# Kernel optimization log

Measured on AMD Instinct MI355X. Metric: run time of the kernel, lower is better.

## Reference

```python
import jax, jax.numpy as jnp
import numpy as np

K = 3        # kernel_size
GROUP = 32   # group
EPS = 1e-5   # BatchNorm eps


def setup_inputs() -> dict:
    key = jax.random.key(0)
    k1, k2 = jax.random.split(key)
    x = jax.random.normal(k1, (4, 256, 128, 128), jnp.float32)
    conv_w = jax.random.normal(k2, (GROUP * K * K, 256, K, K), jnp.float32) * 0.05
    gamma = jnp.ones((GROUP * K * K,), jnp.float32)
    beta = jnp.zeros((GROUP * K * K,), jnp.float32)
    return {"x": x, "conv_w": conv_w, "gamma": gamma, "beta": beta}


def _bilinear_align_corners(x, H, W):
    # F.upsample(..., mode='bilinear', align_corners=True)
    n, c, h, w = x.shape
    ys = jnp.linspace(0.0, h - 1.0, H)
    xs = jnp.linspace(0.0, w - 1.0, W)
    y0 = jnp.floor(ys).astype(jnp.int32)
    x0 = jnp.floor(xs).astype(jnp.int32)
    y1 = jnp.minimum(y0 + 1, h - 1)
    x1 = jnp.minimum(x0 + 1, w - 1)
    wy = (ys - y0)[None, None, :, None]
    wx = (xs - x0)[None, None, None, :]
    rows0 = x[:, :, y0, :]
    rows1 = x[:, :, y1, :]
    top = rows0[:, :, :, x0] * (1 - wx) + rows0[:, :, :, x1] * wx
    bot = rows1[:, :, :, x0] * (1 - wx) + rows1[:, :, :, x1] * wx
    return top * (1 - wy) + bot * wy


def reference(x, conv_w, gamma, beta):
    n, c, h0, w0 = x.shape
    # sigma = softmax(BN(conv(x))) over the full G*K*K channel dim
    sigma = jax.lax.conv_general_dilated(
        x, conv_w, (1, 1), 'VALID', dimension_numbers=('NCHW', 'OIHW', 'NCHW'))
    mean = sigma.mean(axis=(0, 2, 3))
    var = sigma.var(axis=(0, 2, 3))  # biased, matches BN training mode
    sigma = (sigma - mean[None, :, None, None]) * jax.lax.rsqrt(var + EPS)[None, :, None, None]
    sigma = sigma * gamma[None, :, None, None] + beta[None, :, None, None]
    sigma = jax.nn.softmax(sigma, axis=1)  # (n, G*K*K, h, w)
    h, w = sigma.shape[2], sigma.shape[3]  # h = h0-K+1, w = w0-K+1
    # Unfold: patches (n, c, K*K, h, w) with channel outer, kernel-pos inner (torch F.unfold order)
    patches = jnp.stack([x[:, :, i:i + h, j:j + w]
                         for i in range(K) for j in range(K)], axis=2)
    patches = patches.reshape(n, GROUP, c // GROUP, K * K, h, w)
    sig = sigma.reshape(n, GROUP, K * K, h, w)
    # Per-pixel, per-group weighted sum over the K*K window
    out = jnp.einsum('ngcphw,ngphw->ngchw', patches, sig).reshape(n, c, h, w)
    return _bilinear_align_corners(out, h0, w0)
```

## Files before the change

### kernel.cpp

```cpp
#include <hip/hip_runtime.h>
#include <hip/hip_bf16.h>
#include <math.h>

#define N 4
#define C 256
#define H 128
#define W 128
#define CO 288
#define OH 126
#define OW 126
#define GROUP 32
#define CPG 8
#define EPS 1e-5f

#define HW (OH*OW)
#define XSLICE (H*W)
#define XNSTRIDE (C*H*W)
#define SNSTRIDE (CO*HW)
#define LONSTRIDE (C*HW)
#define WSTRIDE (CO*256)
#define WTOT (9*CO*256)
#define XTOT (N*H*W*C)

typedef unsigned short u16;
typedef __attribute__((ext_vector_type(8))) short short8;
typedef __attribute__((ext_vector_type(4))) float float4v;

__device__ inline u16 f2bf(float v) {
    __hip_bfloat16 b = __float2bfloat16(v);
    return __builtin_bit_cast(u16, b);
}
__device__ inline float bf2f(u16 u) {
    __hip_bfloat16 b = __builtin_bit_cast(__hip_bfloat16, u);
    return __bfloat162float(b);
}

__global__ __launch_bounds__(256) void split_x_kernel(const float* __restrict__ x,
                                                      u16* __restrict__ xh,
                                                      u16* __restrict__ xl) {
    const int ci = threadIdx.x;
    const int w0 = blockIdx.x * 8;
    const int h  = blockIdx.y;
    const int n  = blockIdx.z;
    const float* src = x + ((size_t)(n*C + ci)*H + h)*W + w0;
    float4 v0 = *(const float4*)src;
    float4 v1 = *(const float4*)(src + 4);
    float vals[8] = {v0.x, v0.y, v0.z, v0.w, v1.x, v1.y, v1.z, v1.w};
    size_t obase = ((size_t)(n*H + h)*W + w0)*C + ci;
    #pragma unroll
    for (int dw = 0; dw < 8; ++dw) {
        float v = vals[dw];
        u16 hb = f2bf(v);
        xh[obase + (size_t)dw*C] = hb;
        xl[obase + (size_t)dw*C] = f2bf(v - bf2f(hb));
    }
}

__global__ __launch_bounds__(256) void split_w_kernel(const float* __restrict__ wgt,
                                                      u16* __restrict__ whT,
                                                      u16* __restrict__ wlT) {
    const int i = blockIdx.x*256 + threadIdx.x;
    const int ci = i & 255;
    const int co = (i >> 8) % CO;
    const int s  = i / (CO*256);
    float v = wgt[(size_t)co*(C*9) + (size_t)ci*9 + s];
    u16 hb = f2bf(v);
    whT[i] = hb;
    wlT[i] = f2bf(v - bf2f(hb));
}

__global__ __launch_bounds__(256, 2) void conv_mfma_kernel(const u16* __restrict__ xh,
                                                           const u16* __restrict__ whT,
                                                           float* __restrict__ sigma) {
    __shared__ __align__(16) u16 xs[8*4*66*8];
    __shared__ __align__(16) u16 wsh[2*4*288*8];

    const int tid  = threadIdx.x;
    const int wave = tid >> 6;
    const int lane = tid & 63;
    const int m16  = lane & 15;
    const int q    = lane >> 4;
    const int wr   = wave & 1;
    const int wc   = wave >> 1;
    const int ow0  = blockIdx.x * 64;
    const int oh0  = blockIdx.y * 2;
    const int n    = blockIdx.z;

    const int bid = blockIdx.x + 2*(blockIdx.y + 63*blockIdx.z);
    if (bid & 1) __builtin_amdgcn_s_sleep(40);

    const int w_nw   = (wave < 2) ? 5 : 4;
    const int w_base = (wave < 2) ? wave*320 : 640 + (wave-2)*256;
    int wsrc[5];
    #pragma unroll
    for (int i = 0; i < 5; ++i) {
        int c = w_base + i*64 + lane;
        const int cq  = c / 288;
        const int cco = c - cq*288;
        wsrc[i] = cco*256 + cq*8;
    }

    int xoff[9];
    #pragma unroll
    for (int t = 0; t < 9; ++t) {
        int c = (4*t + wave)*64 + lane;
        if (c > 2111) c = 2111;
        const int spq = c / 264;
        const int rem = c - spq*264;
        const int row = rem / 66;
        const int col = rem - row*66;
        int gc = ow0 + col; if (gc > W-1) gc = W-1;
        xoff[t] = (spq >> 2)*XTOT + ((n*H + oh0 + row)*W + gc)*C + (spq & 3)*8;
    }

    const int aoff = (q*264 + wr*66 + m16)*8;
    const int boff = (q*288 + wc*144 + m16)*8;

    float4v acc[4][9];
    #pragma unroll
    for (int mt = 0; mt < 4; ++mt)
        #pragma unroll
        for (int j = 0; j < 9; ++j) acc[mt][j] = (float4v)(0.f);

    #pragma unroll
    for (int t = 0; t < 9; ++t)
        if (t < 8 || wave == 0)
            __builtin_amdgcn_global_load_lds((const uint*)(xh + xoff[t]),
                                             (uint*)(xs + (4*t + wave)*512), 16, 0, 0);
    #pragma unroll
    for (int i = 0; i < 5; ++i)
        if (i < w_nw)
            __builtin_amdgcn_global_load_lds((const uint*)(whT + wsrc[i]),
                                             (uint*)(wsh + (w_base + i*64)*8), 16, 0, 0);
    __syncthreads();

    int buf = 0;
    for (int ci0 = 0; ci0 < C; ci0 += 32) {
        #pragma unroll
        for (int ky = 0; ky < 3; ++ky)
        #pragma unroll
        for (int kx = 0; kx < 3; ++kx) {
            const int s = ky*3 + kx;

            {
                const int soff = WTOT + s*WSTRIDE + ci0;
                #pragma unroll
                for (int i = 0; i < 5; ++i)
                    if (i < w_nw)
                        __builtin_amdgcn_global_load_lds(
                            (const uint*)(whT + soff + wsrc[i]),
                            (uint*)(wsh + ((buf^1)*1152 + w_base + i*64)*8), 16, 0, 0);
            }
            const int ab = aoff + (ky*66 + kx)*8;
            short8 ah0 = *(const short8*)&xs[ab];
            short8 ah1 = *(const short8*)&xs[ab + 128];
            short8 ah2 = *(const short8*)&xs[ab + 256];
            short8 ah3 = *(const short8*)&xs[ab + 384];
            {
                short8 al0 = *(const short8*)&xs[ab + 8448];
                short8 al1 = *(const short8*)&xs[ab + 8448 + 128];
                short8 al2 = *(const short8*)&xs[ab + 8448 + 256];
                short8 al3 = *(const short8*)&xs[ab + 8448 + 384];
                const u16* wb = wsh + buf*9216 + boff;
                __builtin_amdgcn_s_setprio(1);
                #pragma unroll
                for (int j = 0; j < 9; ++j) {
                    short8 bh = *(const short8*)&wb[j*128];
                    acc[0][j] = __builtin_amdgcn_mfma_f32_16x16x32_bf16(ah0, bh, acc[0][j], 0, 0, 0);
                    acc[1][j] = __builtin_amdgcn_mfma_f32_16x16x32_bf16(ah1, bh, acc[1][j], 0, 0, 0);
                    acc[2][j] = __builtin_amdgcn_mfma_f32_16x16x32_bf16(ah2, bh, acc[2][j], 0, 0, 0);
                    acc[3][j] = __builtin_amdgcn_mfma_f32_16x16x32_bf16(ah3, bh, acc[3][j], 0, 0, 0);
                    acc[0][j] = __builtin_amdgcn_mfma_f32_16x16x32_bf16(al0, bh, acc[0][j], 0, 0, 0);
                    acc[1][j] = __builtin_amdgcn_mfma_f32_16x16x32_bf16(al1, bh, acc[1][j], 0, 0, 0);
                    acc[2][j] = __builtin_amdgcn_mfma_f32_16x16x32_bf16(al2, bh, acc[2][j], 0, 0, 0);
                    acc[3][j] = __builtin_amdgcn_mfma_f32_16x16x32_bf16(al3, bh, acc[3][j], 0, 0, 0);
                }
                __builtin_amdgcn_s_setprio(0);
            }
            __syncthreads();
            buf ^= 1;

            if (!(ci0 == C-32 && s == 8)) {
                int ns = s + 1, nci = ci0;
                if (ns == 9) { ns = 0; nci += 32; }
                const int soff = ns*WSTRIDE + nci;
                #pragma unroll
                for (int i = 0; i < 5; ++i)
                    if (i < w_nw)
                        __builtin_amdgcn_global_load_lds(
                            (const uint*)(whT + soff + wsrc[i]),
                            (uint*)(wsh + ((buf^1)*1152 + w_base + i*64)*8), 16, 0, 0);
                if (s == 8) {
                    #pragma unroll
                    for (int t = 0; t < 9; ++t)
                        if (t < 8 || wave == 0)
                            __builtin_amdgcn_global_load_lds(
                                (const uint*)(xh + xoff[t] + nci),
                                (uint*)(xs + (4*t + wave)*512), 16, 0, 0);
                }
            }
            {
                const u16* wb = wsh + buf*9216 + boff;
                __builtin_amdgcn_s_setprio(1);
                #pragma unroll
                for (int j = 0; j < 9; ++j) {
                    short8 bl = *(const short8*)&wb[j*128];
                    acc[0][j] = __builtin_amdgcn_mfma_f32_16x16x32_bf16(ah0, bl, acc[0][j], 0, 0, 0);
                    acc[1][j] = __builtin_amdgcn_mfma_f32_16x16x32_bf16(ah1, bl, acc[1][j], 0, 0, 0);
                    acc[2][j] = __builtin_amdgcn_mfma_f32_16x16x32_bf16(ah2, bl, acc[2][j], 0, 0, 0);
                    acc[3][j] = __builtin_amdgcn_mfma_f32_16x16x32_bf16(ah3, bl, acc[3][j], 0, 0, 0);
                }
                __builtin_amdgcn_s_setprio(0);
            }
            __syncthreads();
            buf ^= 1;
        }
    }

    #pragma unroll
    for (int mt = 0; mt < 4; ++mt) {
        const int posb = mt*16 + q*4;
        #pragma unroll
        for (int j = 0; j < 9; ++j) {
            const int co = wc*144 + j*16 + m16;
            float* dst = sigma + (size_t)n*SNSTRIDE + (size_t)co*HW + (oh0 + wr)*OW;
            #pragma unroll
            for (int r = 0; r < 4; ++r) {
                const int ow = ow0 + posb + r;
                if (ow < OW) dst[ow] = acc[mt][j][r];
            }
        }
    }
}

__global__ __launch_bounds__(1024) void stats_kernel(const float* __restrict__ sigma,
                                                     const float* __restrict__ gamma,
                                                     const float* __restrict__ beta,
                                                     float* __restrict__ coef) {
    const int c = blockIdx.x;
    float sum = 0.f, sq = 0.f;
    for (int n = 0; n < N; ++n) {
        const float* sp = sigma + (size_t)n*SNSTRIDE + (size_t)c*HW;
        for (int i = threadIdx.x; i < HW; i += 1024) {
            float v = sp[i];
            sum += v; sq += v * v;
        }
    }
    for (int off = 32; off > 0; off >>= 1) {
        sum += __shfl_down(sum, off, 64);
        sq  += __shfl_down(sq,  off, 64);
    }
    __shared__ float ls[16], lq[16];
    const int wid = threadIdx.x >> 6, lane = threadIdx.x & 63;
    if (lane == 0) { ls[wid] = sum; lq[wid] = sq; }
    __syncthreads();
    if (threadIdx.x == 0) {
        float S = 0.f, Q = 0.f;
        #pragma unroll
        for (int i = 0; i < 16; ++i) { S += ls[i]; Q += lq[i]; }
        const float cnt = (float)(N * HW);
        float mean = S / cnt;
        float var  = Q / cnt - mean * mean;
        float a = gamma[c] * rsqrtf(var + EPS);
        coef[c]      = a;
        coef[CO + c] = beta[c] - mean * a;
    }
}

__global__ __launch_bounds__(256) void fuse_kernel(const float* __restrict__ x,
                                                   const float* __restrict__ sigma,
                                                   const float* __restrict__ coef,
                                                   float* __restrict__ outlo,
                                                   float* __restrict__ sums) {
    __shared__ float a[CO], b[CO];
    for (int i = threadIdx.x; i < CO; i += 256) {
        a[i] = coef[i];
        b[i] = coef[CO + i];
    }
    __syncthreads();

    const int t4 = blockIdx.x * 256 + threadIdx.x;
    if (t4 >= N * HW * 4) return;
    const int gpos = t4 >> 2;
    const int gc   = t4 & 3;
    const int n  = gpos / HW;
    const int hw = gpos - n * HW;
    const int oh = hw / OW;
    const int ow = hw - oh * OW;

    const float* sp = sigma + (size_t)n * SNSTRIDE + hw;
    const float* xb = x + (size_t)n * XNSTRIDE + oh * W + ow;
    float* ob = outlo + (size_t)n * LONSTRIDE + hw;

    float sum = 0.f;
    for (int gl = 0; gl < 8; ++gl) {
        const int g = gc * 8 + gl;
        float acc[CPG];
        #pragma unroll
        for (int c = 0; c < CPG; ++c) acc[c] = 0.f;
        #pragma unroll
        for (int p = 0; p < 9; ++p) {
            const int ch = g * 9 + p;
            float s = sp[(size_t)ch * HW] * a[ch] + b[ch];
            float e = __expf(s);
            sum += e;
            const float* xr = xb + (size_t)(g * CPG) * XSLICE + (p / 3) * W + (p % 3);
            #pragma unroll
            for (int c = 0; c < CPG; ++c)
                acc[c] += xr[(size_t)c * XSLICE] * e;
        }
        #pragma unroll
        for (int c = 0; c < CPG; ++c)
            ob[(size_t)(g * CPG + c) * HW] = acc[c];
    }
    sum += __shfl_xor(sum, 1, 64);
    sum += __shfl_xor(sum, 2, 64);
    if (gc == 0) sums[gpos] = sum;
}

__global__ __launch_bounds__(256) void upsample_kernel(const float* __restrict__ lo,
                                                       const float* __restrict__ sums,
                                                       float* __restrict__ out) {
    const int idx = blockIdx.x * 256 + threadIdx.x;
    const int xi = idx & (W - 1);
    const int yi = (idx >> 7) & (H - 1);
    const int nc = idx >> 14;
    const int n  = nc >> 8;

    const float scale = 125.0f / 127.0f;
    const float sy = yi * scale;
    const float sx = xi * scale;
    int y0 = (int)sy;
    int x0 = (int)sx;
    float wy = sy - (float)y0;
    float wx = sx - (float)x0;
    int y1 = min(y0 + 1, OH - 1);
    int x1 = min(x0 + 1, OW - 1);

    const float* p  = lo + (size_t)nc * HW;
    const float* ps = sums + (size_t)n * HW;
    float v00 = p[y0 * OW + x0] / ps[y0 * OW + x0];
    float v01 = p[y0 * OW + x1] / ps[y0 * OW + x1];
    float v10 = p[y1 * OW + x0] / ps[y1 * OW + x0];
    float v11 = p[y1 * OW + x1] / ps[y1 * OW + x1];
    float top = v00 * (1.f - wx) + v01 * wx;
    float bot = v10 * (1.f - wx) + v11 * wx;
    out[idx] = top * (1.f - wy) + bot * wy;
}

extern "C" void kernel_launch(void* const* d_in, const int* in_sizes, int n_in,
                              void* d_out, int out_size, void* d_ws, size_t ws_size,
                              hipStream_t stream) {
    const float* x      = (const float*)d_in[0];
    const float* conv_w = (const float*)d_in[1];
    const float* gamma  = (const float*)d_in[2];
    const float* beta   = (const float*)d_in[3];
    float* out = (float*)d_out;
    float* ws  = (float*)d_ws;

    float* sigma = ws;
    float* coef  = ws + 18289152;
    float* outlo = ws + 18290176;
    u16* xhp = (u16*)(ws + 18290176);
    u16* xlp = xhp + (size_t)XTOT;
    u16* whT = xlp + (size_t)XTOT;
    u16* wlT = whT + (size_t)WTOT;
    float* sums = (float*)whT;

    split_x_kernel<<<dim3(16, 128, 4), 256, 0, stream>>>(x, xhp, xlp);
    split_w_kernel<<<(9*CO*256)/256, 256, 0, stream>>>(conv_w, whT, wlT);

    conv_mfma_kernel<<<dim3(2, 63, N), 256, 0, stream>>>(xhp, whT, sigma);

    stats_kernel<<<CO, 1024, 0, stream>>>(sigma, gamma, beta, coef);

    fuse_kernel<<<(N * HW * 4 + 255) / 256, 256, 0, stream>>>(x, sigma, coef, outlo, sums);

    upsample_kernel<<<(N * C * H * W) / 256, 256, 0, stream>>>(outlo, sums, out);
}
```

Measured before the change: 614.8 us.

## Enlarge conv tile to four output rows with 512-thread blocks and merged weight staging

The conv MFMA kernel now uses 8 waves per block and covers 4 output rows instead of 2, so each weight tile staged in LDS is reused across twice as many pixels. The weight hi and lo halves are loaded together into one larger double buffer, which cuts the barriers per kernel tap from two to one. The tap loop is no longer unrolled, and the staggered s_sleep start is dropped. In exchange the kernel needs much more LDS per block (about 125 KB), which limits occupancy. Padded rows are clamped on load and skipped on store.

```diff
diff --git a/kernel.cpp b/kernel.cpp
--- a/kernel.cpp
+++ b/kernel.cpp
@@ -69,51 +69,51 @@
     wlT[i] = f2bf(v - bf2f(hb));
 }
 
-__global__ __launch_bounds__(256, 2) void conv_mfma_kernel(const u16* __restrict__ xh,
+__global__ __launch_bounds__(512, 2) void conv_mfma_kernel(const u16* __restrict__ xh,
                                                            const u16* __restrict__ whT,
                                                            float* __restrict__ sigma) {
-    __shared__ __align__(16) u16 xs[8*4*66*8];
-    __shared__ __align__(16) u16 wsh[2*4*288*8];
+    __shared__ __align__(16) u16 xs[25600];
+    __shared__ __align__(16) u16 wsh[2*18432];
 
     const int tid  = threadIdx.x;
     const int wave = tid >> 6;
     const int lane = tid & 63;
     const int m16  = lane & 15;
     const int q    = lane >> 4;
-    const int wr   = wave & 1;
-    const int wc   = wave >> 1;
+    const int wr   = wave & 3;
+    const int wc   = wave >> 2;
     const int ow0  = blockIdx.x * 64;
-    const int oh0  = blockIdx.y * 2;
+    const int oh0  = blockIdx.y * 4;
     const int n    = blockIdx.z;
 
-    const int bid = blockIdx.x + 2*(blockIdx.y + 63*blockIdx.z);
-    if (bid & 1) __builtin_amdgcn_s_sleep(40);
-
-    const int w_nw   = (wave < 2) ? 5 : 4;
-    const int w_base = (wave < 2) ? wave*320 : 640 + (wave-2)*256;
+    const int w_n    = (wave < 4) ? 5 : 4;
+    const int w_base = (wave < 4) ? wave*320 : 1280 + (wave-4)*256;
     int wsrc[5];
     #pragma unroll
     for (int i = 0; i < 5; ++i) {
         int c = w_base + i*64 + lane;
-        const int cq  = c / 288;
-        const int cco = c - cq*288;
-        wsrc[i] = cco*256 + cq*8;
-    }
-
-    int xoff[9];
-    #pragma unroll
-    for (int t = 0; t < 9; ++t) {
-        int c = (4*t + wave)*64 + lane;
-        if (c > 2111) c = 2111;
-        const int spq = c / 264;
-        const int rem = c - spq*264;
+        const int sp  = c / 1152;
+        const int rem = c - sp*1152;
+        const int qc  = rem / 288;
+        const int co  = rem - qc*288;
+        wsrc[i] = sp*WTOT + co*256 + qc*8;
+    }
+
+    int xoff[7];
+    #pragma unroll
+    for (int t = 0; t < 7; ++t) {
+        int c = (8*t + wave)*64 + lane;
+        if (c > 3167) c = 3167;
+        const int spq = c / 396;
+        const int rem = c - spq*396;
         const int row = rem / 66;
         const int col = rem - row*66;
+        int gr = oh0 + row; if (gr > H-1) gr = H-1;
         int gc = ow0 + col; if (gc > W-1) gc = W-1;
-        xoff[t] = (spq >> 2)*XTOT + ((n*H + oh0 + row)*W + gc)*C + (spq & 3)*8;
-    }
-
-    const int aoff = (q*264 + wr*66 + m16)*8;
+        xoff[t] = (spq >> 2)*XTOT + ((n*H + gr)*W + gc)*C + (spq & 3)*8;
+    }
+
+    const int aoff = (q*396 + wr*66 + m16)*8;
     const int boff = (q*288 + wc*144 + m16)*8;
 
     float4v acc[4][9];
@@ -123,111 +123,105 @@
         for (int j = 0; j < 9; ++j) acc[mt][j] = (float4v)(0.f);
 
     #pragma unroll
-    for (int t = 0; t < 9; ++t)
-        if (t < 8 || wave == 0)
+    for (int t = 0; t < 7; ++t)
+        if (t < 6 || wave < 2)
             __builtin_amdgcn_global_load_lds((const uint*)(xh + xoff[t]),
-                                             (uint*)(xs + (4*t + wave)*512), 16, 0, 0);
+                                             (uint*)(xs + (8*t + wave)*512), 16, 0, 0);
     #pragma unroll
     for (int i = 0; i < 5; ++i)
-        if (i < w_nw)
+        if (i < w_n)
             __builtin_amdgcn_global_load_lds((const uint*)(whT + wsrc[i]),
                                              (uint*)(wsh + (w_base + i*64)*8), 16, 0, 0);
     __syncthreads();
 
     int buf = 0;
     for (int ci0 = 0; ci0 < C; ci0 += 32) {
-        #pragma unroll
-        for (int ky = 0; ky < 3; ++ky)
-        #pragma unroll
-        for (int kx = 0; kx < 3; ++kx) {
-            const int s = ky*3 + kx;
-
-            {
-                const int soff = WTOT + s*WSTRIDE + ci0;
+        #pragma unroll 1
+        for (int s = 0; s < 9; ++s) {
+            if (s < 8) {
+                const int soff = (s+1)*WSTRIDE + ci0;
                 #pragma unroll
                 for (int i = 0; i < 5; ++i)
-                    if (i < w_nw)
+                    if (i < w_n)
                         __builtin_amdgcn_global_load_lds(
                             (const uint*)(whT + soff + wsrc[i]),
-                            (uint*)(wsh + ((buf^1)*1152 + w_base + i*64)*8), 16, 0, 0);
-            }
+                            (uint*)(wsh + ((buf^1)*18432 + (w_base + i*64)*8)), 16, 0, 0);
+            }
+
+            const int ky = s / 3;
+            const int kx = s - 3*ky;
             const int ab = aoff + (ky*66 + kx)*8;
             short8 ah0 = *(const short8*)&xs[ab];
             short8 ah1 = *(const short8*)&xs[ab + 128];
             short8 ah2 = *(const short8*)&xs[ab + 256];
             short8 ah3 = *(const short8*)&xs[ab + 384];
-            {
-                short8 al0 = *(const short8*)&xs[ab + 8448];
-                short8 al1 = *(const short8*)&xs[ab + 8448 + 128];
-                short8 al2 = *(const short8*)&xs[ab + 8448 + 256];
-                short8 al3 = *(const short8*)&xs[ab + 8448 + 384];
-                const u16* wb = wsh + buf*9216 + boff;
-                __builtin_amdgcn_s_setprio(1);
-                #pragma unroll
-                for (int j = 0; j < 9; ++j) {
-                    short8 bh = *(const short8*)&wb[j*128];
-                    acc[0][j] = __builtin_amdgcn_mfma_f32_16x16x32_bf16(ah0, bh, acc[0][j], 0, 0, 0);
-                    acc[1][j] = __builtin_amdgcn_mfma_f32_16x16x32_bf16(ah1, bh, acc[1][j], 0, 0, 0);
-                    acc[2][j] = __builtin_amdgcn_mfma_f32_16x16x32_bf16(ah2, bh, acc[2][j], 0, 0, 0);
-                    acc[3][j] = __builtin_amdgcn_mfma_f32_16x16x32_bf16(ah3, bh, acc[3][j], 0, 0, 0);
-                    acc[0][j] = __builtin_amdgcn_mfma_f32_16x16x32_bf16(al0, bh, acc[0][j], 0, 0, 0);
-                    acc[1][j] = __builtin_amdgcn_mfma_f32_16x16x32_bf16(al1, bh, acc[1][j], 0, 0, 0);
-                    acc[2][j] = __builtin_amdgcn_mfma_f32_16x16x32_bf16(al2, bh, acc[2][j], 0, 0, 0);
-                    acc[3][j] = __builtin_amdgcn_mfma_f32_16x16x32_bf16(al3, bh, acc[3][j], 0, 0, 0);
-                }
-                __builtin_amdgcn_s_setprio(0);
-            }
-            __syncthreads();
-            buf ^= 1;
-
-            if (!(ci0 == C-32 && s == 8)) {
-                int ns = s + 1, nci = ci0;
-                if (ns == 9) { ns = 0; nci += 32; }
-                const int soff = ns*WSTRIDE + nci;
-                #pragma unroll
-                for (int i = 0; i < 5; ++i)
-                    if (i < w_nw)
-                        __builtin_amdgcn_global_load_lds(
-                            (const uint*)(whT + soff + wsrc[i]),
-                            (uint*)(wsh + ((buf^1)*1152 + w_base + i*64)*8), 16, 0, 0);
-                if (s == 8) {
+            short8 al0 = *(const short8*)&xs[ab + 12672];
+            short8 al1 = *(const short8*)&xs[ab + 12672 + 128];
+            short8 al2 = *(const short8*)&xs[ab + 12672 + 256];
+            short8 al3 = *(const short8*)&xs[ab + 12672 + 384];
+
+            if (s == 8) {
+                __syncthreads();
+                const int nci = ci0 + 32;
+                if (nci < C) {
                     #pragma unroll
-                    for (int t = 0; t < 9; ++t)
-                        if (t < 8 || wave == 0)
+                    for (int t = 0; t < 7; ++t)
+                        if (t < 6 || wave < 2)
                             __builtin_amdgcn_global_load_lds(
                                 (const uint*)(xh + xoff[t] + nci),
-                                (uint*)(xs + (4*t + wave)*512), 16, 0, 0);
+                                (uint*)(xs + (8*t + wave)*512), 16, 0, 0);
+                    #pragma unroll
+                    for (int i = 0; i < 5; ++i)
+                        if (i < w_n)
+                            __builtin_amdgcn_global_load_lds(
+                                (const uint*)(whT + nci + wsrc[i]),
+                                (uint*)(wsh + ((buf^1)*18432 + (w_base + i*64)*8)), 16, 0, 0);
                 }
             }
-            {
-                const u16* wb = wsh + buf*9216 + boff;
-                __builtin_amdgcn_s_setprio(1);
-                #pragma unroll
-                for (int j = 0; j < 9; ++j) {
-                    short8 bl = *(const short8*)&wb[j*128];
-                    acc[0][j] = __builtin_amdgcn_mfma_f32_16x16x32_bf16(ah0, bl, acc[0][j], 0, 0, 0);
-                    acc[1][j] = __builtin_amdgcn_mfma_f32_16x16x32_bf16(ah1, bl, acc[1][j], 0, 0, 0);
-                    acc[2][j] = __builtin_amdgcn_mfma_f32_16x16x32_bf16(ah2, bl, acc[2][j], 0, 0, 0);
-                    acc[3][j] = __builtin_amdgcn_mfma_f32_16x16x32_bf16(ah3, bl, acc[3][j], 0, 0, 0);
-                }
-                __builtin_amdgcn_s_setprio(0);
-            }
+
+            const u16* wb = wsh + buf*18432 + boff;
+            __builtin_amdgcn_s_setprio(1);
+            #pragma unroll
+            for (int j = 0; j < 9; ++j) {
+                short8 bh = *(const short8*)&wb[j*128];
+                acc[0][j] = __builtin_amdgcn_mfma_f32_16x16x32_bf16(ah0, bh, acc[0][j], 0, 0, 0);
+                acc[1][j] = __builtin_amdgcn_mfma_f32_16x16x32_bf16(ah1, bh, acc[1][j], 0, 0, 0);
+                acc[2][j] = __builtin_amdgcn_mfma_f32_16x16x32_bf16(ah2, bh, acc[2][j], 0, 0, 0);
+                acc[3][j] = __builtin_amdgcn_mfma_f32_16x16x32_bf16(ah3, bh, acc[3][j], 0, 0, 0);
+                acc[0][j] = __builtin_amdgcn_mfma_f32_16x16x32_bf16(al0, bh, acc[0][j], 0, 0, 0);
+                acc[1][j] = __builtin_amdgcn_mfma_f32_16x16x32_bf16(al1, bh, acc[1][j], 0, 0, 0);
+                acc[2][j] = __builtin_amdgcn_mfma_f32_16x16x32_bf16(al2, bh, acc[2][j], 0, 0, 0);
+                acc[3][j] = __builtin_amdgcn_mfma_f32_16x16x32_bf16(al3, bh, acc[3][j], 0, 0, 0);
+            }
+            #pragma unroll
+            for (int j = 0; j < 9; ++j) {
+                short8 bl = *(const short8*)&wb[9216 + j*128];
+                acc[0][j] = __builtin_amdgcn_mfma_f32_16x16x32_bf16(ah0, bl, acc[0][j], 0, 0, 0);
+                acc[1][j] = __builtin_amdgcn_mfma_f32_16x16x32_bf16(ah1, bl, acc[1][j], 0, 0, 0);
+                acc[2][j] = __builtin_amdgcn_mfma_f32_16x16x32_bf16(ah2, bl, acc[2][j], 0, 0, 0);
+                acc[3][j] = __builtin_amdgcn_mfma_f32_16x16x32_bf16(ah3, bl, acc[3][j], 0, 0, 0);
+            }
+            __builtin_amdgcn_s_setprio(0);
+
             __syncthreads();
             buf ^= 1;
         }
     }
 
-    #pragma unroll
-    for (int mt = 0; mt < 4; ++mt) {
-        const int posb = mt*16 + q*4;
-        #pragma unroll
-        for (int j = 0; j < 9; ++j) {
-            const int co = wc*144 + j*16 + m16;
-            float* dst = sigma + (size_t)n*SNSTRIDE + (size_t)co*HW + (oh0 + wr)*OW;
+    const int oh = oh0 + wr;
+    if (oh < OH) {
+        #pragma unroll
+        for (int mt = 0; mt < 4; ++mt) {
+            const int posb = mt*16 + q*4;
             #pragma unroll
-            for (int r = 0; r < 4; ++r) {
-                const int ow = ow0 + posb + r;
-                if (ow < OW) dst[ow] = acc[mt][j][r];
+            for (int j = 0; j < 9; ++j) {
+                const int co = wc*144 + j*16 + m16;
+                float* dst = sigma + (size_t)n*SNSTRIDE + (size_t)co*HW + oh*OW;
+                #pragma unroll
+                for (int r = 0; r < 4; ++r) {
+                    const int ow = ow0 + posb + r;
+                    if (ow < OW) dst[ow] = acc[mt][j][r];
+                }
             }
         }
     }
@@ -370,7 +364,7 @@
     split_x_kernel<<<dim3(16, 128, 4), 256, 0, stream>>>(x, xhp, xlp);
     split_w_kernel<<<(9*CO*256)/256, 256, 0, stream>>>(conv_w, whT, wlT);
 
-    conv_mfma_kernel<<<dim3(2, 63, N), 256, 0, stream>>>(xhp, whT, sigma);
+    conv_mfma_kernel<<<dim3(2, 32, N), 512, 0, stream>>>(xhp, whT, sigma);
 
     stats_kernel<<<CO, 1024, 0, stream>>>(sigma, gamma, beta, coef);
 
```

Measured after the change: 596.3 us. 1.03x faster.
